# Performance work log

Measured on AMD Instinct MI355X. Metric: run time of the kernel, lower is better.

Reference implementation:

```python
import jax, jax.numpy as jnp
import numpy as np

NQ = 8          # qubits -> 2^8 = 256 amplitudes
B = 32768       # batch

# ---- gate matrices (torchquantum conventions) ----

def _rx(t):
    c = jnp.cos(t / 2).astype(jnp.complex64)
    s = jnp.sin(t / 2).astype(jnp.complex64)
    return jnp.stack([jnp.stack([c, -1j * s]), jnp.stack([-1j * s, c])])

def _ry(t):
    c = jnp.cos(t / 2).astype(jnp.complex64)
    s = jnp.sin(t / 2).astype(jnp.complex64)
    return jnp.stack([jnp.stack([c, -s]), jnp.stack([s, c])])

def _rz(t):
    tc = t.astype(jnp.complex64)
    z = jnp.zeros((), jnp.complex64)
    return jnp.stack([jnp.stack([jnp.exp(-0.5j * tc), z]),
                      jnp.stack([z, jnp.exp(0.5j * tc)])])

def _u3(p):
    th, ph, lm = p[0], p[1], p[2]
    ct = jnp.cos(th / 2).astype(jnp.complex64)
    st = jnp.sin(th / 2).astype(jnp.complex64)
    eip = jnp.exp(1j * ph.astype(jnp.complex64))
    eil = jnp.exp(1j * lm.astype(jnp.complex64))
    return jnp.stack([jnp.stack([ct, -eil * st]),
                      jnp.stack([eip * st, eip * eil * ct])])

# ---- statevector ops; state shape [B] + [2]*NQ ----

def apply_1q(state, U, w):
    s = jnp.moveaxis(state, 1 + w, -1)
    s = jnp.einsum('ij,b...j->b...i', U, s)
    return jnp.moveaxis(s, -1, 1 + w)

def apply_ctrl(state, U, c, t):
    s = jnp.moveaxis(state, (1 + c, 1 + t), (-2, -1))
    s1 = jnp.einsum('ij,b...j->b...i', U, s[..., 1, :])
    s = jnp.concatenate([s[..., :1, :], s1[..., None, :]], axis=-2)
    return jnp.moveaxis(s, (-2, -1), (1 + c, 1 + t))

def expval_z(state, w):
    p = state.real ** 2 + state.imag ** 2
    axes = tuple(i for i in range(1, NQ + 1) if i != 1 + w)
    pm = jnp.sum(p, axis=axes)  # [B, 2]
    return pm[:, 0] - pm[:, 1]

def encode(x):
    # RY angle encoding: product state, amplitude per qubit = (cos(x/2), sin(x/2))
    a = jnp.stack([jnp.cos(x / 2), jnp.sin(x / 2)], -1).astype(jnp.complex64)  # [B,8,2]
    state = a[:, 0]
    for q in range(1, NQ):
        state = jnp.einsum('b...i,bj->b...ij', state, a[:, q])
    return state  # [B,2,2,...,2]

CR_PAIRS_1 = [(0, 1), (2, 3), (4, 5), (6, 7), (1, 2), (3, 4), (5, 6)]
CR_PAIRS_2 = [(1, 3), (5, 7), (3, 5)]

def branch(state, cr_fn, crp, u3p):
    # crp: [10] angles, u3p: [6,3]
    for i, (c, t) in enumerate(CR_PAIRS_1):
        state = apply_ctrl(state, cr_fn(crp[i]), c, t)
    # intermediate tqm.expval calls do not mutate the state -> omitted
    for i, w in enumerate([1, 3, 5, 7]):
        state = apply_1q(state, _u3(u3p[i]), w)
    for i, (c, t) in enumerate(CR_PAIRS_2):
        state = apply_ctrl(state, cr_fn(crp[7 + i]), c, t)
    state = apply_1q(state, _u3(u3p[4]), 3)
    state = apply_1q(state, _u3(u3p[5]), 7)
    return jnp.stack([expval_z(state, 3), expval_z(state, 7)], axis=1)  # [B,2]


def setup_inputs() -> dict:
    key = jax.random.key(0)
    ks = jax.random.split(key, 12)
    pi = np.float32(np.pi)
    u = lambda k, shape: jax.random.uniform(k, shape, jnp.float32, -pi, pi)
    return {
        'x': u(ks[0], (B, NQ)),
        'crx_params': u(ks[1], (10,)),
        'u3x_params': u(ks[2], (6, 3)),
        'cry_params': u(ks[3], (10,)),
        'u3y_params': u(ks[4], (6, 3)),
        'crz_params': u(ks[5], (10,)),
        'u3z_params': u(ks[6], (6, 3)),
        'w1': jax.random.normal(ks[7], (12, 6), jnp.float32) * 0.3,
        'b1': jnp.zeros((12,), jnp.float32),
        'w2': jax.random.normal(ks[8], (1, 12), jnp.float32) * 0.3,
        'b2': jnp.zeros((1,), jnp.float32),
    }


def reference(x, crx_params, u3x_params, cry_params, u3y_params,
              crz_params, u3z_params, w1, b1, w2, b2):
    state = encode(x)
    fx = branch(state, _rx, crx_params, u3x_params)  # CRX branch (qdev)
    fy = branch(state, _ry, cry_params, u3y_params)  # CRY branch (qdev1)
    fz = branch(state, _rz, crz_params, u3z_params)  # CRZ branch (qdev2)
    feats = jnp.concatenate([fx, fy, fz], axis=1)    # [B,6]
    h = jnp.tanh(feats @ w1.T + b1)
    return jax.nn.sigmoid(h @ w2.T + b2)             # [B,1]
```

## Files before the change

kernel.cpp:

```cpp
#include <hip/hip_runtime.h>
#include <math.h>


typedef float v2f __attribute__((ext_vector_type(2)));

__device__ __forceinline__ v2f mk2(float a, float b) { v2f r; r.x = a; r.y = b; return r; }
__device__ __forceinline__ v2f ld2(const float* __restrict__ p) { return *(const v2f*)p; }

__device__ __forceinline__ v2f pk_mul_s(v2f a, v2f b) { v2f d;
  asm("v_pk_mul_f32 %0, %1, %2 op_sel:[0,0] op_sel_hi:[0,1]" : "=v"(d) : "v"(a), "v"(b)); return d; }
__device__ __forceinline__ v2f pk_fma_irot(v2f a, v2f b, v2f c) { v2f d;
  asm("v_pk_fma_f32 %0, %1, %2, %3 op_sel:[1,1,0] op_sel_hi:[1,0,1] neg_lo:[0,1,0]" : "=v"(d) : "v"(a), "v"(b), "v"(c)); return d; }
__device__ __forceinline__ v2f cmul(v2f a, v2f b) { return pk_fma_irot(a, b, pk_mul_s(a, b)); }
__device__ __forceinline__ v2f pk_mul_swap(v2f a, v2f b) { v2f d;
  asm("v_pk_mul_f32 %0, %1, %2 op_sel:[1,0] op_sel_hi:[0,1]" : "=v"(d) : "v"(a), "v"(b)); return d; }

__device__ __forceinline__ v2f pk_mul_sM(v2f M, v2f b) { v2f d;
  asm("v_pk_mul_f32 %0, %1, %2 op_sel:[0,0] op_sel_hi:[0,1]" : "=v"(d) : "s"(M), "v"(b)); return d; }
__device__ __forceinline__ v2f pk_fma_sloM(v2f M, v2f b, v2f c) { v2f d;
  asm("v_pk_fma_f32 %0, %1, %2, %3 op_sel:[0,0,0] op_sel_hi:[0,1,1]" : "=v"(d) : "s"(M), "v"(b), "v"(c)); return d; }
__device__ __forceinline__ v2f pk_fma_shiM(v2f M, v2f b, v2f c) { v2f d;
  asm("v_pk_fma_f32 %0, %1, %2, %3 op_sel:[1,0,0] op_sel_hi:[1,1,1]" : "=v"(d) : "s"(M), "v"(b), "v"(c)); return d; }
__device__ __forceinline__ v2f pk_fma_shi_negM(v2f M, v2f b, v2f c) { v2f d;
  asm("v_pk_fma_f32 %0, %1, %2, %3 op_sel:[1,0,0] op_sel_hi:[1,1,1] neg_lo:[1,0,0] neg_hi:[1,0,0]" : "=v"(d) : "s"(M), "v"(b), "v"(c)); return d; }
__device__ __forceinline__ v2f pk_fma_rotM(v2f M, v2f b, v2f c) { v2f d;
  asm("v_pk_fma_f32 %0, %1, %2, %3 op_sel:[1,1,0] op_sel_hi:[1,0,1] neg_hi:[0,1,0]" : "=v"(d) : "s"(M), "v"(b), "v"(c)); return d; }
__device__ __forceinline__ v2f pk_fma_irotM(v2f M, v2f b, v2f c) { v2f d;
  asm("v_pk_fma_f32 %0, %1, %2, %3 op_sel:[1,1,0] op_sel_hi:[1,0,1] neg_lo:[0,1,0]" : "=v"(d) : "s"(M), "v"(b), "v"(c)); return d; }

template <int MASK>
__device__ __forceinline__ float shuf1(float v) {
  if constexpr (MASK == 1) {
    return __int_as_float(__builtin_amdgcn_mov_dpp(__float_as_int(v), 0xB1, 0xf, 0xf, true));
  } else if constexpr (MASK == 2) {
    return __int_as_float(__builtin_amdgcn_mov_dpp(__float_as_int(v), 0x4E, 0xf, 0xf, true));
  } else {
    constexpr int pat = (MASK << 10) | 0x1F;
    return __int_as_float(__builtin_amdgcn_ds_swizzle(__float_as_int(v), pat));
  }
}
template <int MASK>
__device__ __forceinline__ v2f shuf2(v2f v) {
  v2f r; r.x = shuf1<MASK>(v.x); r.y = shuf1<MASK>(v.y); return r;
}

template <bool A_REAL>
__device__ __forceinline__ v2f u3row_s(v2f ua, v2f ub, v2f a, v2f b) {
  v2f t = pk_mul_sM(ua, a);
  if constexpr (!A_REAL) t = pk_fma_irotM(ua, a, t);
  t = pk_fma_sloM(ub, b, t);
  return pk_fma_irotM(ub, b, t);
}

template <int SB>
__device__ __forceinline__ void u3_apply(v2f w[32], const float* __restrict__ p) {
  const v2f M0 = ld2(p), M1 = ld2(p + 2), M2 = ld2(p + 4), M3 = ld2(p + 6);
#pragma unroll
  for (int i = 0; i < 32; ++i) {
    if (i & (1 << SB)) continue;
    const int i1 = i | (1 << SB);
    const v2f a = w[i], b = w[i1];
    w[i] = u3row_s<true>(M0, M1, a, b);
    w[i1] = u3row_s<false>(M3, M2, b, a);
  }
}

template <int SB, int CB, bool M00R>
__device__ __forceinline__ void u3_sel(v2f w[32], const float* __restrict__ pM,
                                       const float* __restrict__ pN) {
  const v2f M0 = ld2(pM), M1 = ld2(pM + 2), M2 = ld2(pM + 4), M3 = ld2(pM + 6);
  const v2f N0 = ld2(pN), N1 = ld2(pN + 2), N2 = ld2(pN + 4), N3 = ld2(pN + 6);
#pragma unroll
  for (int i = 0; i < 32; ++i) {
    if (i & (1 << SB)) continue;
    const int i1 = i | (1 << SB);
    const v2f a = w[i], b = w[i1];
    if ((i >> CB) & 1) {
      w[i] = u3row_s<false>(N0, N1, a, b);
      w[i1] = u3row_s<false>(N3, N2, b, a);
    } else {
      w[i] = u3row_s<M00R>(M0, M1, a, b);
      w[i1] = u3row_s<false>(M3, M2, b, a);
    }
  }
}

template <int SB, int LB>
__device__ __forceinline__ void crx_Sc_Lt(v2f w[32], v2f cs) {
#pragma unroll
  for (int i = 0; i < 32; ++i) {
    if (!(i & (1 << SB))) continue;
    const v2f p = shuf2<(1 << LB)>(w[i]);
    w[i] = pk_fma_rotM(cs, p, pk_mul_sM(cs, w[i]));
  }
}

template <int SB, int LB>
__device__ __forceinline__ void cr_ry_r(float w[32], v2f cs, int gl) {
  const bool tb = (gl >> LB) & 1;
  const float Ky = tb ? cs.y : -cs.y;
#pragma unroll
  for (int i = 0; i < 32; ++i) {
    if (!(i & (1 << SB))) continue;
    const float p = shuf1<(1 << LB)>(w[i]);
    w[i] = __builtin_fmaf(Ky, p, cs.x * w[i]);
  }
}

template <int KIND, int SBc, int SBt>
__device__ __forceinline__ void cr_Sc_St(v2f w[32], v2f cs) {
#pragma unroll
  for (int i = 0; i < 32; ++i) {
    if (!(i & (1 << SBc))) continue;
    if constexpr (KIND == 2) {
      const v2f t = pk_mul_sM(cs, w[i]);
      w[i] = (i & (1 << SBt)) ? pk_fma_irotM(cs, w[i], t)
                              : pk_fma_rotM(cs, w[i], t);
    } else {
      if (i & (1 << SBt)) continue;
      const int i1 = i | (1 << SBt);
      const v2f a = w[i], b = w[i1];
      if constexpr (KIND == 0) {
        w[i] = pk_fma_rotM(cs, b, pk_mul_sM(cs, a));
        w[i1] = pk_fma_rotM(cs, a, pk_mul_sM(cs, b));
      } else {
        w[i] = pk_fma_shi_negM(cs, b, pk_mul_sM(cs, a));
        w[i1] = pk_fma_shiM(cs, a, pk_mul_sM(cs, b));
      }
    }
  }
}

template <int SB>
__device__ __forceinline__ void u3_lift(v2f w[32], const float wr[32],
                                        const float* __restrict__ p) {
  const v2f M0 = ld2(p), M1 = ld2(p + 2), M2 = ld2(p + 4), M3 = ld2(p + 6);
#pragma unroll
  for (int i = 0; i < 32; ++i) {
    if (i & (1 << SB)) continue;
    const int i1 = i | (1 << SB);
    const float a = wr[i], b = wr[i1];
    w[i] = mk2(__builtin_fmaf(a, M0.x, b * M1.x), b * M1.y);
    w[i1] = mk2(__builtin_fmaf(a, M2.x, b * M3.x),
                __builtin_fmaf(a, M2.y, b * M3.y));
  }
}

__device__ __forceinline__ void measure2(v2f w[32], const float* __restrict__ q,
                                         v2f res[2]) {
  const v2f qa = ld2(q);
  const v2f qg = ld2(q + 2);
  float z3[2], z7[2];
#pragma unroll
  for (int e = 0; e < 2; ++e) {
    float z3a = 0.f, z3b = 0.f, z7p = 0.f, z7m = 0.f;
#pragma unroll
    for (int s0 = 0; s0 < 16; s0 += 2) {
      const v2f a = w[e * 16 + s0], b = w[e * 16 + s0 + 1];
      const v2f t1 = a * b, t2 = pk_mul_swap(a, b), t3 = a * a, t4 = b * b;
      const float r = t1.x + t1.y;
      const float m = t2.x - t2.y;
      const float na = t3.x + t3.y;
      const float nb = t4.x + t4.y;
      z3a = __builtin_fmaf(qa.x, na, z3a);
      z3b = __builtin_fmaf(qa.y, nb, z3b);
      z3a = __builtin_fmaf(qg.x, r, z3a);
      z3b = __builtin_fmaf(-qg.y, m, z3b);
      const float nn = na + nb;
      if (s0 & 2) z7m += nn; else z7p += nn;
    }
    z3[e] = z3a + z3b;
    z7[e] = z7p - z7m;
  }
  z3[0] += shuf1<1>(z3[0]); z3[1] += shuf1<1>(z3[1]); z7[0] += shuf1<1>(z7[0]); z7[1] += shuf1<1>(z7[1]);
  z3[0] += shuf1<2>(z3[0]); z3[1] += shuf1<2>(z3[1]); z7[0] += shuf1<2>(z7[0]); z7[1] += shuf1<2>(z7[1]);
  z3[0] += shuf1<4>(z3[0]); z3[1] += shuf1<4>(z3[1]); z7[0] += shuf1<4>(z7[0]); z7[1] += shuf1<4>(z7[1]);
  z3[0] += shuf1<8>(z3[0]); z3[1] += shuf1<8>(z3[1]); z7[0] += shuf1<8>(z7[0]); z7[1] += shuf1<8>(z7[1]);
  res[0] = mk2(z3[0], z7[0]);
  res[1] = mk2(z3[1], z7[1]);
}

template <int KIND>
__device__ __forceinline__ void tail_common(v2f w[32], const float* __restrict__ Gb,
                                            v2f res[2]) {
  u3_sel<0, 3, true>(w, Gb + 72, Gb + 80);
  u3_apply<2>(w, Gb + 88);
  u3_sel<1, 2, false>(w, Gb + 96, Gb + 104);
  cr_Sc_St<KIND, 0, 2>(w, ld2(Gb + 56));
  measure2(w, Gb + 112, res);
}

__device__ __forceinline__ void load_sincos(const float* __restrict__ xb,
                                            float sn[8], float cn[8]) {
  const float4 xlo = ((const float4*)xb)[0];
  const float4 xhi = ((const float4*)xb)[1];
  const float xq[8] = {xlo.x, xlo.y, xlo.z, xlo.w, xhi.x, xhi.y, xhi.z, xhi.w};
#pragma unroll
  for (int q = 0; q < 8; ++q) __sincosf(0.5f * xq[q], &sn[q], &cn[q]);
}

__device__ __forceinline__ void run_rx(const float* __restrict__ xb0,
                                       const float* __restrict__ xb1,
                                       const float* __restrict__ Gb, int gl,
                                       v2f res[2]) {
  const bool l0 = gl & 1, l1 = (gl >> 1) & 1, l2 = (gl >> 2) & 1, l3 = (gl >> 3) & 1;
  v2f w[32];
#pragma unroll
  for (int e = 0; e < 2; ++e) {
    float sn[8], cn[8];
    load_sincos(e ? xb1 : xb0, sn, cn);
    v2f pa[4], pb[4];
#pragma unroll
    for (int pr = 0; pr < 4; ++pr) {
      const bool lh = (pr == 0) ? l0 : (pr == 1) ? l1 : (pr == 2) ? l2 : l3;
      const float c = Gb[pr * 8], s = Gb[pr * 8 + 1];
      const float uc = lh ? sn[2 * pr] : cn[2 * pr];
      const float b0 = uc * cn[2 * pr + 1], b1 = uc * sn[2 * pr + 1];
      const float Kx = lh ? c : 1.f;
      const float Kyn = lh ? -s : 0.f;
      pa[pr] = mk2(Kx * b0, Kyn * b1);
      pb[pr] = mk2(Kx * b1, Kyn * b0);
    }
    v2f A[4] = {cmul(pa[0], pa[2]), cmul(pa[0], pb[2]), cmul(pb[0], pa[2]), cmul(pb[0], pb[2])};
    v2f Bv[4] = {cmul(pa[3], pa[1]), cmul(pa[3], pb[1]), cmul(pb[3], pa[1]), cmul(pb[3], pb[1])};
#pragma unroll
    for (int s = 0; s < 16; ++s) w[e * 16 + s] = cmul(A[s >> 2], Bv[s & 3]);
  }
  crx_Sc_Lt<3, 1>(w, ld2(Gb + 32));
  crx_Sc_Lt<0, 2>(w, ld2(Gb + 40));
  crx_Sc_Lt<2, 3>(w, ld2(Gb + 48));
  u3_apply<3>(w, Gb + 64);
  tail_common<0>(w, Gb, res);
}

__device__ __forceinline__ void run_ry(const float* __restrict__ xb0,
                                       const float* __restrict__ xb1,
                                       const float* __restrict__ Gb, int gl,
                                       v2f res[2]) {
  const bool l0 = gl & 1, l1 = (gl >> 1) & 1, l2 = (gl >> 2) & 1, l3 = (gl >> 3) & 1;
  float wr[32];
#pragma unroll
  for (int e = 0; e < 2; ++e) {
    float sn[8], cn[8];
    load_sincos(e ? xb1 : xb0, sn, cn);
    float pa[4], pb[4];
#pragma unroll
    for (int pr = 0; pr < 4; ++pr) {
      const bool lh = (pr == 0) ? l0 : (pr == 1) ? l1 : (pr == 2) ? l2 : l3;
      const float c = Gb[pr * 8], s = Gb[pr * 8 + 1];
      const float uc = lh ? sn[2 * pr] : cn[2 * pr];
      const float b0 = uc * cn[2 * pr + 1], b1 = uc * sn[2 * pr + 1];
      const float Kx = lh ? c : 1.f;
      const float Ky = lh ? s : 0.f;
      pa[pr] = Kx * b0 - Ky * b1;
      pb[pr] = Ky * b0 + Kx * b1;
    }
    const float A[4] = {pa[0] * pa[2], pa[0] * pb[2], pb[0] * pa[2], pb[0] * pb[2]};
    const float Bv[4] = {pa[3] * pa[1], pa[3] * pb[1], pb[3] * pa[1], pb[3] * pb[1]};
#pragma unroll
    for (int s = 0; s < 16; ++s) wr[e * 16 + s] = A[s >> 2] * Bv[s & 3];
  }
  cr_ry_r<3, 1>(wr, ld2(Gb + 32), gl);
  cr_ry_r<0, 2>(wr, ld2(Gb + 40), gl);
  cr_ry_r<2, 3>(wr, ld2(Gb + 48), gl);
  v2f w[32];
  u3_lift<3>(w, wr, Gb + 64);
  tail_common<1>(w, Gb, res);
}

__device__ __forceinline__ void run_rz(const float* __restrict__ xb0,
                                       const float* __restrict__ xb1,
                                       const float* __restrict__ Gb, int gl,
                                       v2f res[2]) {
  const bool l0 = gl & 1, l1 = (gl >> 1) & 1, l2 = (gl >> 2) & 1, l3 = (gl >> 3) & 1;
  const float t0 = Gb[2], h0 = Gb[3];
  const float t1 = Gb[10], h1 = Gb[11];
  const float t2 = Gb[18], h2 = Gb[19];
  const float t3 = Gb[26], h3 = Gb[27];
  const float h4 = Gb[35], h5 = Gb[43], h6 = Gb[51];
  const float kk0 = (l1 ? t1 : 0.f) + (l2 ? h5 : -h5);
  const float kk1 = (l3 ? t3 : 0.f);
  const float kk2 = (l2 ? t2 : 0.f) + (l3 ? h6 : -h6);
  const float kk3 = (l0 ? t0 : 0.f) + (l1 ? h4 : -h4);
  const float aa = -((l0 ? h0 : 0.f) + (l1 ? h1 : 0.f) + (l2 ? h2 : 0.f) + (l3 ? h3 : 0.f));
  float v01[2][4], v23[2][4];
#pragma unroll
  for (int e = 0; e < 2; ++e) {
    float sn[8], cn[8];
    load_sincos(e ? xb1 : xb0, sn, cn);
    const float u0 = l0 ? sn[0] : cn[0];
    const float u2 = l1 ? sn[2] : cn[2];
    const float u4 = l2 ? sn[4] : cn[4];
    const float u6 = l3 ? sn[6] : cn[6];
    const float P = (u0 * u2) * (u4 * u6);
    v01[e][0] = P * (cn[3] * cn[7]); v01[e][1] = P * (sn[3] * cn[7]);
    v01[e][2] = P * (cn[3] * sn[7]); v01[e][3] = P * (sn[3] * sn[7]);
    v23[e][0] = cn[5] * cn[1]; v23[e][1] = sn[5] * cn[1];
    v23[e][2] = cn[5] * sn[1]; v23[e][3] = sn[5] * sn[1];
  }
  v2f w[32];
#pragma unroll
  for (int s = 0; s < 16; ++s) {
    float phv = aa;
    if (s & 1) phv += kk0;
    if (s & 2) phv += kk1;
    if (s & 4) phv += kk2;
    if (s & 8) phv += kk3;
    float sp, cp;
    __sincosf(phv, &sp, &cp);
    const float e0 = v01[0][s & 3] * v23[0][s >> 2];
    const float e1 = v01[1][s & 3] * v23[1][s >> 2];
    w[s] = mk2(e0 * cp, e0 * sp);
    w[16 + s] = mk2(e1 * cp, e1 * sp);
  }
  u3_apply<3>(w, Gb + 64);
  tail_common<2>(w, Gb, res);
}

struct c2 { float r, i; };
__device__ __forceinline__ c2 cmulh(c2 a, c2 b) { return {a.r * b.r - a.i * b.i, a.r * b.i + a.i * b.r}; }
__device__ __forceinline__ c2 cmulc(c2 a, c2 b) { return {a.r * b.r + a.i * b.i, a.i * b.r - a.r * b.i}; }
__device__ __forceinline__ c2 caddh(c2 a, c2 b) { return {a.r + b.r, a.i + b.i}; }
__device__ void mat2mul(const c2 A[4], const c2 B[4], c2 C[4]) {
  C[0] = caddh(cmulh(A[0], B[0]), cmulh(A[1], B[2]));
  C[1] = caddh(cmulh(A[0], B[1]), cmulh(A[1], B[3]));
  C[2] = caddh(cmulh(A[2], B[0]), cmulh(A[3], B[2]));
  C[3] = caddh(cmulh(A[2], B[1]), cmulh(A[3], B[3]));
}
__device__ void u3m(const float* p, c2 M[4]) {
  float st, ct, sp, cp, sl, cl;
  sincosf(0.5f * p[0], &st, &ct);
  sincosf(p[1], &sp, &cp);
  sincosf(p[2], &sl, &cl);
  M[0] = {ct, 0.f};
  M[1] = {-cl * st, -sl * st};
  M[2] = {cp * st, sp * st};
  M[3] = {(cp * cl - sp * sl) * ct, (sp * cl + cp * sl) * ct};
}
__device__ void rmat(int kind, float th, c2 R[4]) {
  float s, c;
  sincosf(0.5f * th, &s, &c);
  if (kind == 0) { R[0] = {c, 0.f}; R[1] = {0.f, -s}; R[2] = {0.f, -s}; R[3] = {c, 0.f}; }
  else if (kind == 1) { R[0] = {c, 0.f}; R[1] = {-s, 0.f}; R[2] = {s, 0.f}; R[3] = {c, 0.f}; }
  else { R[0] = {c, -s}; R[1] = {0.f, 0.f}; R[2] = {0.f, 0.f}; R[3] = {c, s}; }
}
__device__ void storeM(float* dst, const c2 M[4]) {
#pragma unroll
  for (int j = 0; j < 4; ++j) { dst[2 * j] = M[j].r; dst[2 * j + 1] = M[j].i; }
}

__global__ void qcnn_prep(const float* __restrict__ crx, const float* __restrict__ u3x,
                          const float* __restrict__ cry, const float* __restrict__ u3y,
                          const float* __restrict__ crz, const float* __restrict__ u3z,
                          float* __restrict__ G) {
  const int br = threadIdx.x;
  if (br >= 3) return;
  const float* crp = (br == 0) ? crx : (br == 1) ? cry : crz;
  const float* u3p = (br == 0) ? u3x : (br == 1) ? u3y : u3z;
  float* Gb = G + br * 128;

  const int crIdx[8] = {0, 1, 2, 3, 4, 5, 6, 9};
#pragma unroll
  for (int i = 0; i < 8; ++i) {
    const float th = crp[crIdx[i]];
    float s, c;
    sincosf(0.5f * th, &s, &c);
    Gb[i * 8] = c;
    Gb[i * 8 + 1] = s;
    Gb[i * 8 + 2] = th;
    Gb[i * 8 + 3] = 0.5f * th;
  }
  c2 U1v[4], U3v[4], U5v[4], U7a[4], U7b[4], U3f[4], R[4], T[4], T2[4];
  u3m(u3p + 0, U1v);
  u3m(u3p + 3, U3v);
  u3m(u3p + 6, U5v);
  u3m(u3p + 9, U7a);
  u3m(u3p + 12, U3f);
  u3m(u3p + 15, U7b);
  storeM(Gb + 64, U1v);
  storeM(Gb + 72, U3v);
  rmat(br, crp[7], R);
  mat2mul(R, U3v, T);
  storeM(Gb + 80, T);
  storeM(Gb + 88, U5v);
  mat2mul(U7b, U7a, T);
  storeM(Gb + 96, T);
  rmat(br, crp[8], R);
  mat2mul(R, U7a, T);
  mat2mul(U7b, T, T2);
  storeM(Gb + 104, T2);
  const float n00 = U3f[0].r * U3f[0].r + U3f[0].i * U3f[0].i;
  const float n01 = U3f[1].r * U3f[1].r + U3f[1].i * U3f[1].i;
  const float n10 = U3f[2].r * U3f[2].r + U3f[2].i * U3f[2].i;
  const float n11 = U3f[3].r * U3f[3].r + U3f[3].i * U3f[3].i;
  const c2 g01 = cmulc(U3f[0], U3f[1]);
  const c2 g23 = cmulc(U3f[2], U3f[3]);
  Gb[112] = n00 - n10;
  Gb[113] = n01 - n11;
  Gb[114] = 2.f * (g01.r - g23.r);
  Gb[115] = 2.f * (g01.i - g23.i);
}

__global__ __launch_bounds__(256) void qcnn_main(
    const float* __restrict__ x, const float* __restrict__ G,
    const float* __restrict__ w1, const float* __restrict__ b1,
    const float* __restrict__ w2, const float* __restrict__ b2,
    float* __restrict__ out, int B) {
  const int gid = blockIdx.x * blockDim.x + threadIdx.x;
  const int grp = gid >> 4;
  const int gl = threadIdx.x & 15;
  const int b0 = grp * 2;
  if (b0 >= B) return;
  const float* xb0 = x + b0 * 8;
  const float* xb1 = x + (b0 + 1) * 8;

  v2f fx[2], fy[2], fz[2];
  run_rx(xb0, xb1, G, gl, fx);
  run_ry(xb0, xb1, G + 128, gl, fy);
  run_rz(xb0, xb1, G + 256, gl, fz);

  const int j = (gl < 12) ? gl : 0;
  const float* w1r = w1 + j * 6;
  const float w10 = w1r[0], w11 = w1r[1], w12 = w1r[2];
  const float w13 = w1r[3], w14 = w1r[4], w15 = w1r[5];
  const float b1v = b1[j], w2v = w2[j], b2v = b2[0];
  float a0 = b1v + w10 * fx[0].x + w11 * fx[0].y + w12 * fy[0].x +
             w13 * fy[0].y + w14 * fz[0].x + w15 * fz[0].y;
  float a1 = b1v + w10 * fx[1].x + w11 * fx[1].y + w12 * fy[1].x +
             w13 * fy[1].y + w14 * fz[1].x + w15 * fz[1].y;
  const float e0 = __expf(2.f * a0), e1 = __expf(2.f * a1);
  const float th0 = 1.f - 2.f * __builtin_amdgcn_rcpf(e0 + 1.f);
  const float th1 = 1.f - 2.f * __builtin_amdgcn_rcpf(e1 + 1.f);
  float t0 = (gl < 12) ? w2v * th0 : 0.f;
  float t1 = (gl < 12) ? w2v * th1 : 0.f;
  t0 += shuf1<1>(t0); t1 += shuf1<1>(t1);
  t0 += shuf1<2>(t0); t1 += shuf1<2>(t1);
  t0 += shuf1<4>(t0); t1 += shuf1<4>(t1);
  t0 += shuf1<8>(t0); t1 += shuf1<8>(t1);
  const float r0 = __builtin_amdgcn_rcpf(1.f + __expf(-(t0 + b2v)));
  const float r1 = __builtin_amdgcn_rcpf(1.f + __expf(-(t1 + b2v)));
  if (gl == 0) {
    out[b0] = r0;
    out[b0 + 1] = r1;
  }
}

extern "C" void kernel_launch(void* const* d_in, const int* in_sizes, int n_in,
                              void* d_out, int out_size, void* d_ws,
                              size_t ws_size, hipStream_t stream) {
  const float* x = (const float*)d_in[0];
  const float* crx = (const float*)d_in[1];
  const float* u3x = (const float*)d_in[2];
  const float* cry = (const float*)d_in[3];
  const float* u3y = (const float*)d_in[4];
  const float* crz = (const float*)d_in[5];
  const float* u3z = (const float*)d_in[6];
  const float* w1 = (const float*)d_in[7];
  const float* b1 = (const float*)d_in[8];
  const float* w2 = (const float*)d_in[9];
  const float* b2 = (const float*)d_in[10];
  float* out = (float*)d_out;
  float* G = (float*)d_ws;
  const int B = in_sizes[0] / 8;

  hipLaunchKernelGGL(qcnn_prep, dim3(1), dim3(64), 0, stream, crx, u3x, cry,
                     u3y, crz, u3z, G);
  const int ngroups = (B + 1) / 2;
  const int threads = 256;
  const int blocks = (ngroups * 16 + threads - 1) / threads;
  hipLaunchKernelGGL(qcnn_main, dim3(blocks), dim3(threads), 0, stream, x, G,
                     w1, b1, w2, b2, out, B);
}
```

Before: 106.5 us.

## Fold gate-matrix prep kernel into main kernel with per-wave recompute

Removes the separate single-block prep kernel that built gate matrices into a workspace buffer. Each thread now computes the sincos values and fused 2x2 unitaries itself and broadcasts them to scalar registers via readfirstlane, so there is one launch and no dependent workspace loads. The cost is redundant transcendental and matrix math in every wavefront, a switch from sincosf to the lower-accuracy __sincosf, and more register pressure.

```diff
diff --git a/kernel.cpp b/kernel.cpp
--- a/kernel.cpp
+++ b/kernel.cpp
@@ -5,7 +5,6 @@
 typedef float v2f __attribute__((ext_vector_type(2)));
 
 __device__ __forceinline__ v2f mk2(float a, float b) { v2f r; r.x = a; r.y = b; return r; }
-__device__ __forceinline__ v2f ld2(const float* __restrict__ p) { return *(const v2f*)p; }
 
 __device__ __forceinline__ v2f pk_mul_s(v2f a, v2f b) { v2f d;
   asm("v_pk_mul_f32 %0, %1, %2 op_sel:[0,0] op_sel_hi:[0,1]" : "=v"(d) : "v"(a), "v"(b)); return d; }
@@ -44,6 +43,89 @@
   v2f r; r.x = shuf1<MASK>(v.x); r.y = shuf1<MASK>(v.y); return r;
 }
 
+__device__ __forceinline__ float rflf(float v) {
+  return __int_as_float(__builtin_amdgcn_readfirstlane(__float_as_int(v)));
+}
+__device__ __forceinline__ v2f rfl2(float a, float b) { return mk2(rflf(a), rflf(b)); }
+
+struct c2 { float r, i; };
+__device__ __forceinline__ c2 cmulh(c2 a, c2 b) { return {a.r * b.r - a.i * b.i, a.r * b.i + a.i * b.r}; }
+__device__ __forceinline__ c2 cmulc(c2 a, c2 b) { return {a.r * b.r + a.i * b.i, a.i * b.r - a.r * b.i}; }
+__device__ __forceinline__ c2 caddh(c2 a, c2 b) { return {a.r + b.r, a.i + b.i}; }
+__device__ __forceinline__ void mat2mul(const c2 A[4], const c2 B[4], c2 C[4]) {
+  C[0] = caddh(cmulh(A[0], B[0]), cmulh(A[1], B[2]));
+  C[1] = caddh(cmulh(A[0], B[1]), cmulh(A[1], B[3]));
+  C[2] = caddh(cmulh(A[2], B[0]), cmulh(A[3], B[2]));
+  C[3] = caddh(cmulh(A[2], B[1]), cmulh(A[3], B[3]));
+}
+__device__ __forceinline__ void u3mf(float p0, float p1, float p2, c2 M[4]) {
+  float st, ct, sp, cp, sl, cl;
+  __sincosf(0.5f * p0, &st, &ct);
+  __sincosf(p1, &sp, &cp);
+  __sincosf(p2, &sl, &cl);
+  M[0] = {ct, 0.f};
+  M[1] = {-cl * st, -sl * st};
+  M[2] = {cp * st, sp * st};
+  M[3] = {(cp * cl - sp * sl) * ct, (sp * cl + cp * sl) * ct};
+}
+template <int KIND>
+__device__ __forceinline__ void rmatk(float th, c2 R[4]) {
+  float s, c;
+  __sincosf(0.5f * th, &s, &c);
+  if constexpr (KIND == 0) { R[0] = {c, 0.f}; R[1] = {0.f, -s}; R[2] = {0.f, -s}; R[3] = {c, 0.f}; }
+  else if constexpr (KIND == 1) { R[0] = {c, 0.f}; R[1] = {-s, 0.f}; R[2] = {s, 0.f}; R[3] = {c, 0.f}; }
+  else { R[0] = {c, -s}; R[1] = {0.f, 0.f}; R[2] = {0.f, 0.f}; R[3] = {c, s}; }
+}
+
+struct Mats {
+  v2f cs12, cs34, cs56, cs35;
+  v2f U1[4], M13[4], N13[4], U5[4], M7[4], N7[4];
+  v2f qa, qg;
+};
+__device__ __forceinline__ void store_rfl(v2f dst[4], const c2 M[4]) {
+#pragma unroll
+  for (int j = 0; j < 4; ++j) dst[j] = rfl2(M[j].r, M[j].i);
+}
+
+template <int KIND>
+__device__ __forceinline__ void make_mats(const float* __restrict__ crp,
+                                          const float* __restrict__ u3p, Mats& m) {
+  float s, c;
+  if constexpr (KIND != 2) {
+    __sincosf(0.5f * crp[4], &s, &c); m.cs12 = rfl2(c, s);
+    __sincosf(0.5f * crp[5], &s, &c); m.cs34 = rfl2(c, s);
+    __sincosf(0.5f * crp[6], &s, &c); m.cs56 = rfl2(c, s);
+  }
+  __sincosf(0.5f * crp[9], &s, &c); m.cs35 = rfl2(c, s);
+  c2 A[4], Bm[4], R[4], T[4], T2[4];
+  u3mf(u3p[0], u3p[1], u3p[2], A);
+  store_rfl(m.U1, A);
+  u3mf(u3p[3], u3p[4], u3p[5], A);
+  store_rfl(m.M13, A);
+  rmatk<KIND>(crp[7], R);
+  mat2mul(R, A, T);
+  store_rfl(m.N13, T);
+  u3mf(u3p[6], u3p[7], u3p[8], A);
+  store_rfl(m.U5, A);
+  u3mf(u3p[9], u3p[10], u3p[11], A);
+  u3mf(u3p[15], u3p[16], u3p[17], Bm);
+  mat2mul(Bm, A, T);
+  store_rfl(m.M7, T);
+  rmatk<KIND>(crp[8], R);
+  mat2mul(R, A, T);
+  mat2mul(Bm, T, T2);
+  store_rfl(m.N7, T2);
+  u3mf(u3p[12], u3p[13], u3p[14], A);
+  const float n00 = A[0].r * A[0].r + A[0].i * A[0].i;
+  const float n01 = A[1].r * A[1].r + A[1].i * A[1].i;
+  const float n10 = A[2].r * A[2].r + A[2].i * A[2].i;
+  const float n11 = A[3].r * A[3].r + A[3].i * A[3].i;
+  const c2 g01 = cmulc(A[0], A[1]);
+  const c2 g23 = cmulc(A[2], A[3]);
+  m.qa = rfl2(n00 - n10, n01 - n11);
+  m.qg = rfl2(2.f * (g01.r - g23.r), 2.f * (g01.i - g23.i));
+}
+
 template <bool A_REAL>
 __device__ __forceinline__ v2f u3row_s(v2f ua, v2f ub, v2f a, v2f b) {
   v2f t = pk_mul_sM(ua, a);
@@ -53,34 +135,30 @@
 }
 
 template <int SB>
-__device__ __forceinline__ void u3_apply(v2f w[32], const float* __restrict__ p) {
-  const v2f M0 = ld2(p), M1 = ld2(p + 2), M2 = ld2(p + 4), M3 = ld2(p + 6);
+__device__ __forceinline__ void u3_apply(v2f w[32], const v2f M[4]) {
 #pragma unroll
   for (int i = 0; i < 32; ++i) {
     if (i & (1 << SB)) continue;
     const int i1 = i | (1 << SB);
     const v2f a = w[i], b = w[i1];
-    w[i] = u3row_s<true>(M0, M1, a, b);
-    w[i1] = u3row_s<false>(M3, M2, b, a);
+    w[i] = u3row_s<true>(M[0], M[1], a, b);
+    w[i1] = u3row_s<false>(M[3], M[2], b, a);
   }
 }
 
 template <int SB, int CB, bool M00R>
-__device__ __forceinline__ void u3_sel(v2f w[32], const float* __restrict__ pM,
-                                       const float* __restrict__ pN) {
-  const v2f M0 = ld2(pM), M1 = ld2(pM + 2), M2 = ld2(pM + 4), M3 = ld2(pM + 6);
-  const v2f N0 = ld2(pN), N1 = ld2(pN + 2), N2 = ld2(pN + 4), N3 = ld2(pN + 6);
+__device__ __forceinline__ void u3_sel(v2f w[32], const v2f M[4], const v2f N[4]) {
 #pragma unroll
   for (int i = 0; i < 32; ++i) {
     if (i & (1 << SB)) continue;
     const int i1 = i | (1 << SB);
     const v2f a = w[i], b = w[i1];
     if ((i >> CB) & 1) {
-      w[i] = u3row_s<false>(N0, N1, a, b);
-      w[i1] = u3row_s<false>(N3, N2, b, a);
+      w[i] = u3row_s<false>(N[0], N[1], a, b);
+      w[i1] = u3row_s<false>(N[3], N[2], b, a);
     } else {
-      w[i] = u3row_s<M00R>(M0, M1, a, b);
-      w[i1] = u3row_s<false>(M3, M2, b, a);
+      w[i] = u3row_s<M00R>(M[0], M[1], a, b);
+      w[i1] = u3row_s<false>(M[3], M[2], b, a);
     }
   }
 }
@@ -132,24 +210,19 @@
 }
 
 template <int SB>
-__device__ __forceinline__ void u3_lift(v2f w[32], const float wr[32],
-                                        const float* __restrict__ p) {
-  const v2f M0 = ld2(p), M1 = ld2(p + 2), M2 = ld2(p + 4), M3 = ld2(p + 6);
+__device__ __forceinline__ void u3_lift(v2f w[32], const float wr[32], const v2f M[4]) {
 #pragma unroll
   for (int i = 0; i < 32; ++i) {
     if (i & (1 << SB)) continue;
     const int i1 = i | (1 << SB);
     const float a = wr[i], b = wr[i1];
-    w[i] = mk2(__builtin_fmaf(a, M0.x, b * M1.x), b * M1.y);
-    w[i1] = mk2(__builtin_fmaf(a, M2.x, b * M3.x),
-                __builtin_fmaf(a, M2.y, b * M3.y));
-  }
-}
-
-__device__ __forceinline__ void measure2(v2f w[32], const float* __restrict__ q,
-                                         v2f res[2]) {
-  const v2f qa = ld2(q);
-  const v2f qg = ld2(q + 2);
+    w[i] = mk2(__builtin_fmaf(a, M[0].x, b * M[1].x), b * M[1].y);
+    w[i1] = mk2(__builtin_fmaf(a, M[2].x, b * M[3].x),
+                __builtin_fmaf(a, M[2].y, b * M[3].y));
+  }
+}
+
+__device__ __forceinline__ void measure2(v2f w[32], v2f qa, v2f qg, v2f res[2]) {
   float z3[2], z7[2];
 #pragma unroll
   for (int e = 0; e < 2; ++e) {
@@ -181,13 +254,12 @@
 }
 
 template <int KIND>
-__device__ __forceinline__ void tail_common(v2f w[32], const float* __restrict__ Gb,
-                                            v2f res[2]) {
-  u3_sel<0, 3, true>(w, Gb + 72, Gb + 80);
-  u3_apply<2>(w, Gb + 88);
-  u3_sel<1, 2, false>(w, Gb + 96, Gb + 104);
-  cr_Sc_St<KIND, 0, 2>(w, ld2(Gb + 56));
-  measure2(w, Gb + 112, res);
+__device__ __forceinline__ void tail_common(v2f w[32], const Mats& m, v2f res[2]) {
+  u3_sel<0, 3, true>(w, m.M13, m.N13);
+  u3_apply<2>(w, m.U5);
+  u3_sel<1, 2, false>(w, m.M7, m.N7);
+  cr_Sc_St<KIND, 0, 2>(w, m.cs35);
+  measure2(w, m.qa, m.qg, res);
 }
 
 __device__ __forceinline__ void load_sincos(const float* __restrict__ xb,
@@ -201,8 +273,14 @@
 
 __device__ __forceinline__ void run_rx(const float* __restrict__ xb0,
                                        const float* __restrict__ xb1,
-                                       const float* __restrict__ Gb, int gl,
-                                       v2f res[2]) {
+                                       const float* __restrict__ crp,
+                                       const float* __restrict__ u3p,
+                                       int gl, v2f res[2]) {
+  Mats m;
+  make_mats<0>(crp, u3p, m);
+  float cL[4], sL[4];
+#pragma unroll
+  for (int pr = 0; pr < 4; ++pr) __sincosf(0.5f * crp[pr], &sL[pr], &cL[pr]);
   const bool l0 = gl & 1, l1 = (gl >> 1) & 1, l2 = (gl >> 2) & 1, l3 = (gl >> 3) & 1;
   v2f w[32];
 #pragma unroll
@@ -213,11 +291,10 @@
 #pragma unroll
     for (int pr = 0; pr < 4; ++pr) {
       const bool lh = (pr == 0) ? l0 : (pr == 1) ? l1 : (pr == 2) ? l2 : l3;
-      const float c = Gb[pr * 8], s = Gb[pr * 8 + 1];
       const float uc = lh ? sn[2 * pr] : cn[2 * pr];
       const float b0 = uc * cn[2 * pr + 1], b1 = uc * sn[2 * pr + 1];
-      const float Kx = lh ? c : 1.f;
-      const float Kyn = lh ? -s : 0.f;
+      const float Kx = lh ? cL[pr] : 1.f;
+      const float Kyn = lh ? -sL[pr] : 0.f;
       pa[pr] = mk2(Kx * b0, Kyn * b1);
       pb[pr] = mk2(Kx * b1, Kyn * b0);
     }
@@ -226,17 +303,23 @@
 #pragma unroll
     for (int s = 0; s < 16; ++s) w[e * 16 + s] = cmul(A[s >> 2], Bv[s & 3]);
   }
-  crx_Sc_Lt<3, 1>(w, ld2(Gb + 32));
-  crx_Sc_Lt<0, 2>(w, ld2(Gb + 40));
-  crx_Sc_Lt<2, 3>(w, ld2(Gb + 48));
-  u3_apply<3>(w, Gb + 64);
-  tail_common<0>(w, Gb, res);
+  crx_Sc_Lt<3, 1>(w, m.cs12);
+  crx_Sc_Lt<0, 2>(w, m.cs34);
+  crx_Sc_Lt<2, 3>(w, m.cs56);
+  u3_apply<3>(w, m.U1);
+  tail_common<0>(w, m, res);
 }
 
 __device__ __forceinline__ void run_ry(const float* __restrict__ xb0,
                                        const float* __restrict__ xb1,
-                                       const float* __restrict__ Gb, int gl,
-                                       v2f res[2]) {
+                                       const float* __restrict__ crp,
+                                       const float* __restrict__ u3p,
+                                       int gl, v2f res[2]) {
+  Mats m;
+  make_mats<1>(crp, u3p, m);
+  float cL[4], sL[4];
+#pragma unroll
+  for (int pr = 0; pr < 4; ++pr) __sincosf(0.5f * crp[pr], &sL[pr], &cL[pr]);
   const bool l0 = gl & 1, l1 = (gl >> 1) & 1, l2 = (gl >> 2) & 1, l3 = (gl >> 3) & 1;
   float wr[32];
 #pragma unroll
@@ -247,11 +330,10 @@
 #pragma unroll
     for (int pr = 0; pr < 4; ++pr) {
       const bool lh = (pr == 0) ? l0 : (pr == 1) ? l1 : (pr == 2) ? l2 : l3;
-      const float c = Gb[pr * 8], s = Gb[pr * 8 + 1];
       const float uc = lh ? sn[2 * pr] : cn[2 * pr];
       const float b0 = uc * cn[2 * pr + 1], b1 = uc * sn[2 * pr + 1];
-      const float Kx = lh ? c : 1.f;
-      const float Ky = lh ? s : 0.f;
+      const float Kx = lh ? cL[pr] : 1.f;
+      const float Ky = lh ? sL[pr] : 0.f;
       pa[pr] = Kx * b0 - Ky * b1;
       pb[pr] = Ky * b0 + Kx * b1;
     }
@@ -260,24 +342,25 @@
 #pragma unroll
     for (int s = 0; s < 16; ++s) wr[e * 16 + s] = A[s >> 2] * Bv[s & 3];
   }
-  cr_ry_r<3, 1>(wr, ld2(Gb + 32), gl);
-  cr_ry_r<0, 2>(wr, ld2(Gb + 40), gl);
-  cr_ry_r<2, 3>(wr, ld2(Gb + 48), gl);
+  cr_ry_r<3, 1>(wr, m.cs12, gl);
+  cr_ry_r<0, 2>(wr, m.cs34, gl);
+  cr_ry_r<2, 3>(wr, m.cs56, gl);
   v2f w[32];
-  u3_lift<3>(w, wr, Gb + 64);
-  tail_common<1>(w, Gb, res);
+  u3_lift<3>(w, wr, m.U1);
+  tail_common<1>(w, m, res);
 }
 
 __device__ __forceinline__ void run_rz(const float* __restrict__ xb0,
                                        const float* __restrict__ xb1,
-                                       const float* __restrict__ Gb, int gl,
-                                       v2f res[2]) {
+                                       const float* __restrict__ crp,
+                                       const float* __restrict__ u3p,
+                                       int gl, v2f res[2]) {
+  Mats m;
+  make_mats<2>(crp, u3p, m);
   const bool l0 = gl & 1, l1 = (gl >> 1) & 1, l2 = (gl >> 2) & 1, l3 = (gl >> 3) & 1;
-  const float t0 = Gb[2], h0 = Gb[3];
-  const float t1 = Gb[10], h1 = Gb[11];
-  const float t2 = Gb[18], h2 = Gb[19];
-  const float t3 = Gb[26], h3 = Gb[27];
-  const float h4 = Gb[35], h5 = Gb[43], h6 = Gb[51];
+  const float t0 = crp[0], t1 = crp[1], t2 = crp[2], t3 = crp[3];
+  const float h0 = 0.5f * t0, h1 = 0.5f * t1, h2 = 0.5f * t2, h3 = 0.5f * t3;
+  const float h4 = 0.5f * crp[4], h5 = 0.5f * crp[5], h6 = 0.5f * crp[6];
   const float kk0 = (l1 ? t1 : 0.f) + (l2 ? h5 : -h5);
   const float kk1 = (l3 ? t3 : 0.f);
   const float kk2 = (l2 ? t2 : 0.f) + (l3 ? h6 : -h6);
@@ -313,96 +396,15 @@
     w[s] = mk2(e0 * cp, e0 * sp);
     w[16 + s] = mk2(e1 * cp, e1 * sp);
   }
-  u3_apply<3>(w, Gb + 64);
-  tail_common<2>(w, Gb, res);
-}
-
-struct c2 { float r, i; };
-__device__ __forceinline__ c2 cmulh(c2 a, c2 b) { return {a.r * b.r - a.i * b.i, a.r * b.i + a.i * b.r}; }
-__device__ __forceinline__ c2 cmulc(c2 a, c2 b) { return {a.r * b.r + a.i * b.i, a.i * b.r - a.r * b.i}; }
-__device__ __forceinline__ c2 caddh(c2 a, c2 b) { return {a.r + b.r, a.i + b.i}; }
-__device__ void mat2mul(const c2 A[4], const c2 B[4], c2 C[4]) {
-  C[0] = caddh(cmulh(A[0], B[0]), cmulh(A[1], B[2]));
-  C[1] = caddh(cmulh(A[0], B[1]), cmulh(A[1], B[3]));
-  C[2] = caddh(cmulh(A[2], B[0]), cmulh(A[3], B[2]));
-  C[3] = caddh(cmulh(A[2], B[1]), cmulh(A[3], B[3]));
-}
-__device__ void u3m(const float* p, c2 M[4]) {
-  float st, ct, sp, cp, sl, cl;
-  sincosf(0.5f * p[0], &st, &ct);
-  sincosf(p[1], &sp, &cp);
-  sincosf(p[2], &sl, &cl);
-  M[0] = {ct, 0.f};
-  M[1] = {-cl * st, -sl * st};
-  M[2] = {cp * st, sp * st};
-  M[3] = {(cp * cl - sp * sl) * ct, (sp * cl + cp * sl) * ct};
-}
-__device__ void rmat(int kind, float th, c2 R[4]) {
-  float s, c;
-  sincosf(0.5f * th, &s, &c);
-  if (kind == 0) { R[0] = {c, 0.f}; R[1] = {0.f, -s}; R[2] = {0.f, -s}; R[3] = {c, 0.f}; }
-  else if (kind == 1) { R[0] = {c, 0.f}; R[1] = {-s, 0.f}; R[2] = {s, 0.f}; R[3] = {c, 0.f}; }
-  else { R[0] = {c, -s}; R[1] = {0.f, 0.f}; R[2] = {0.f, 0.f}; R[3] = {c, s}; }
-}
-__device__ void storeM(float* dst, const c2 M[4]) {
-#pragma unroll
-  for (int j = 0; j < 4; ++j) { dst[2 * j] = M[j].r; dst[2 * j + 1] = M[j].i; }
-}
-
-__global__ void qcnn_prep(const float* __restrict__ crx, const float* __restrict__ u3x,
-                          const float* __restrict__ cry, const float* __restrict__ u3y,
-                          const float* __restrict__ crz, const float* __restrict__ u3z,
-                          float* __restrict__ G) {
-  const int br = threadIdx.x;
-  if (br >= 3) return;
-  const float* crp = (br == 0) ? crx : (br == 1) ? cry : crz;
-  const float* u3p = (br == 0) ? u3x : (br == 1) ? u3y : u3z;
-  float* Gb = G + br * 128;
-
-  const int crIdx[8] = {0, 1, 2, 3, 4, 5, 6, 9};
-#pragma unroll
-  for (int i = 0; i < 8; ++i) {
-    const float th = crp[crIdx[i]];
-    float s, c;
-    sincosf(0.5f * th, &s, &c);
-    Gb[i * 8] = c;
-    Gb[i * 8 + 1] = s;
-    Gb[i * 8 + 2] = th;
-    Gb[i * 8 + 3] = 0.5f * th;
-  }
-  c2 U1v[4], U3v[4], U5v[4], U7a[4], U7b[4], U3f[4], R[4], T[4], T2[4];
-  u3m(u3p + 0, U1v);
-  u3m(u3p + 3, U3v);
-  u3m(u3p + 6, U5v);
-  u3m(u3p + 9, U7a);
-  u3m(u3p + 12, U3f);
-  u3m(u3p + 15, U7b);
-  storeM(Gb + 64, U1v);
-  storeM(Gb + 72, U3v);
-  rmat(br, crp[7], R);
-  mat2mul(R, U3v, T);
-  storeM(Gb + 80, T);
-  storeM(Gb + 88, U5v);
-  mat2mul(U7b, U7a, T);
-  storeM(Gb + 96, T);
-  rmat(br, crp[8], R);
-  mat2mul(R, U7a, T);
-  mat2mul(U7b, T, T2);
-  storeM(Gb + 104, T2);
-  const float n00 = U3f[0].r * U3f[0].r + U3f[0].i * U3f[0].i;
-  const float n01 = U3f[1].r * U3f[1].r + U3f[1].i * U3f[1].i;
-  const float n10 = U3f[2].r * U3f[2].r + U3f[2].i * U3f[2].i;
-  const float n11 = U3f[3].r * U3f[3].r + U3f[3].i * U3f[3].i;
-  const c2 g01 = cmulc(U3f[0], U3f[1]);
-  const c2 g23 = cmulc(U3f[2], U3f[3]);
-  Gb[112] = n00 - n10;
-  Gb[113] = n01 - n11;
-  Gb[114] = 2.f * (g01.r - g23.r);
-  Gb[115] = 2.f * (g01.i - g23.i);
+  u3_apply<3>(w, m.U1);
+  tail_common<2>(w, m, res);
 }
 
 __global__ __launch_bounds__(256) void qcnn_main(
-    const float* __restrict__ x, const float* __restrict__ G,
+    const float* __restrict__ x,
+    const float* __restrict__ crx, const float* __restrict__ u3x,
+    const float* __restrict__ cry, const float* __restrict__ u3y,
+    const float* __restrict__ crz, const float* __restrict__ u3z,
     const float* __restrict__ w1, const float* __restrict__ b1,
     const float* __restrict__ w2, const float* __restrict__ b2,
     float* __restrict__ out, int B) {
@@ -415,9 +417,9 @@
   const float* xb1 = x + (b0 + 1) * 8;
 
   v2f fx[2], fy[2], fz[2];
-  run_rx(xb0, xb1, G, gl, fx);
-  run_ry(xb0, xb1, G + 128, gl, fy);
-  run_rz(xb0, xb1, G + 256, gl, fz);
+  run_rx(xb0, xb1, crx, u3x, gl, fx);
+  run_ry(xb0, xb1, cry, u3y, gl, fy);
+  run_rz(xb0, xb1, crz, u3z, gl, fz);
 
   const int j = (gl < 12) ? gl : 0;
   const float* w1r = w1 + j * 6;
@@ -460,14 +462,11 @@
   const float* w2 = (const float*)d_in[9];
   const float* b2 = (const float*)d_in[10];
   float* out = (float*)d_out;
-  float* G = (float*)d_ws;
   const int B = in_sizes[0] / 8;
 
-  hipLaunchKernelGGL(qcnn_prep, dim3(1), dim3(64), 0, stream, crx, u3x, cry,
-                     u3y, crz, u3z, G);
   const int ngroups = (B + 1) / 2;
   const int threads = 256;
   const int blocks = (ngroups * 16 + threads - 1) / threads;
-  hipLaunchKernelGGL(qcnn_main, dim3(blocks), dim3(threads), 0, stream, x, G,
-                     w1, b1, w2, b2, out, B);
-}
+  hipLaunchKernelGGL(qcnn_main, dim3(blocks), dim3(threads), 0, stream, x,
+                     crx, u3x, cry, u3y, crz, u3z, w1, b1, w2, b2, out, B);
+}
```

Measured after the change: 108.2 us. No clear change (+1.6%).
